# Kernel tuning notes

Hardware: AMD Instinct MI355X
Metric: run time of the kernel (lower is better)

## Reference

```python
import jax, jax.numpy as jnp
import numpy as np

B, L, E, H = 2, 2048, 1024, 16
D = E // H  # head_dim = 64


def setup_inputs() -> dict:
    key = jax.random.key(0)
    ks = jax.random.split(key, 9)
    s = 1.0 / np.sqrt(E)
    return {
        "query": jax.random.normal(ks[0], (B, L, E), jnp.float32),
        "key": jax.random.normal(ks[1], (B, L, E), jnp.float32),
        "value": jax.random.normal(ks[2], (B, L, E), jnp.float32),
        # torch Linear weights are [out_features, in_features]
        "Wq": jax.random.uniform(ks[3], (E, E), jnp.float32, -s, s),
        "bq": jnp.zeros((E,), jnp.float32),
        "Wk": jax.random.uniform(ks[4], (E, E), jnp.float32, -s, s),  # k_proj, no bias (add_bias_kv=False)
        "Wv": jax.random.uniform(ks[5], (E, E), jnp.float32, -s, s),  # v_proj, no bias
        "Wo": jax.random.uniform(ks[6], (E, E), jnp.float32, -s, s),
        "bo": jnp.zeros((E,), jnp.float32),
    }


def reference(query, key, value, Wq, bq, Wk, Wv, Wo, bo):
    # Projections (torch Linear: y = x @ W.T + b)
    q = query @ Wq.T + bq          # [B, L, E]
    k = key @ Wk.T                 # [B, L, E]
    v = value @ Wv.T               # [B, L, E]
    # Split heads
    q = q.reshape(B, L, H, D)
    k = k.reshape(B, L, H, D)
    v = v.reshape(B, L, H, D)
    # Scaled dot-product attention; the source's chunked online-softmax
    # computes exactly softmax(q k^T / sqrt(D)) v.
    q = q / jnp.sqrt(jnp.asarray(D, q.dtype))
    scores = jnp.einsum("bqhd,bkhd->bhqk", q, k)      # [B, H, L, L]
    probs = jax.nn.softmax(scores, axis=-1)
    out = jnp.einsum("bhqk,bkhd->bqhd", probs, v)     # [B, L, H, D]
    out = out.reshape(B, L, E)
    return out @ Wo.T + bo
```

## Files before the change

### kernel.cpp

```cpp
#include <hip/hip_runtime.h>

typedef __bf16 bf16;
typedef __bf16 bf16x8 __attribute__((ext_vector_type(8)));
typedef __bf16 bf16x4 __attribute__((ext_vector_type(4)));
typedef float  f32x4  __attribute__((ext_vector_type(4)));

#define MFMA_BF16(a, b, c) __builtin_amdgcn_mfma_f32_16x16x32_bf16((a), (b), (c), 0, 0, 0)


__device__ __forceinline__ void async_load16(const bf16* g, const bf16* l) {
    auto gp = (const __attribute__((address_space(1))) unsigned int*)(unsigned long long)(const void*)g;
    auto lp = (__attribute__((address_space(3))) unsigned int*)(unsigned int)(unsigned long long)(const void*)l;
    __builtin_amdgcn_global_load_lds(gp, lp, 16, 0, 0);
}

__global__ void cvt_bf16_kernel(
    const float* __restrict__ s0, const float* __restrict__ s1, const float* __restrict__ s2,
    const float* __restrict__ s3, const float* __restrict__ s4, const float* __restrict__ s5,
    const float* __restrict__ s6,
    bf16* __restrict__ d0, bf16* __restrict__ d1, bf16* __restrict__ d2,
    bf16* __restrict__ d3, bf16* __restrict__ d4, bf16* __restrict__ d5,
    bf16* __restrict__ d6)
{
    const float* src; bf16* dst; int n;
    switch (blockIdx.y) {
        case 0: src = s0; dst = d0; n = 4194304; break;
        case 1: src = s1; dst = d1; n = 4194304; break;
        case 2: src = s2; dst = d2; n = 4194304; break;
        case 3: src = s3; dst = d3; n = 1048576; break;
        case 4: src = s4; dst = d4; n = 1048576; break;
        case 5: src = s5; dst = d5; n = 1048576; break;
        default: src = s6; dst = d6; n = 1048576; break;
    }
    int i = (blockIdx.x * 256 + threadIdx.x) * 4;
    if (i >= n) return;
    float4 f = *(const float4*)(src + i);
    bf16x4 o;
    o.x = (bf16)f.x; o.y = (bf16)f.y; o.z = (bf16)f.z; o.w = (bf16)f.w;
    *(bf16x4*)(dst + i) = o;
}

__global__ __launch_bounds__(256, 2) void gemm4_kernel(
    const bf16* __restrict__ Aq, const bf16* __restrict__ Ak, const bf16* __restrict__ Av,
    const bf16* __restrict__ Ao,
    const bf16* __restrict__ Wq, const bf16* __restrict__ Wk, const bf16* __restrict__ Wv,
    const bf16* __restrict__ Wo,
    const float* __restrict__ bq, const float* __restrict__ bo,
    bf16* __restrict__ Qs, bf16* __restrict__ Ksw, bf16* __restrict__ Vsw,
    float* __restrict__ out, int zbase)
{
    const int z = zbase + blockIdx.z;
    const bf16 *A, *W;
    if (z == 0)      { A = Aq; W = Wq; }
    else if (z == 1) { A = Ak; W = Wk; }
    else if (z == 2) { A = Av; W = Wv; }
    else             { A = Ao; W = Wo; }

    __shared__ __align__(16) bf16 lA[128 * 32];
    __shared__ __align__(16) bf16 lB[128 * 32];

    const int tid  = threadIdx.x;
    const int w    = tid >> 6;
    const int lane = tid & 63;
    const int lm   = lane & 15;
    const int g    = lane >> 4;
    const int m0   = blockIdx.y * 128;
    const int n0   = blockIdx.x * 128;
    const int wm   = (w & 1) * 64;
    const int wn   = (w >> 1) * 64;

    f32x4 acc[4][4] = {};
    const int sbase = w * 128 + lane;

    for (int kb = 0; kb < 32; kb++) {
        __syncthreads();
#pragma unroll
        for (int t = 0; t < 2; t++) {
            int s   = sbase + t * 64;
            int row = s >> 2;
            int gs  = s & 3;
            int gg  = gs ^ ((row >> 1) & 3);
            const bf16* ga = A + (size_t)(m0 + row) * 1024 + kb * 32 + gg * 8;
            const bf16* gb = W + (size_t)(n0 + row) * 1024 + kb * 32 + gg * 8;
            async_load16(ga, lA + s * 8);
            async_load16(gb, lB + s * 8);
        }
        __syncthreads();

        bf16x8 af[4], bfr[4];
#pragma unroll
        for (int mt = 0; mt < 4; mt++) {
            int row = wm + mt * 16 + lm;
            af[mt] = *(const bf16x8*)(lA + row * 32 + ((g ^ ((row >> 1) & 3)) << 3));
        }
#pragma unroll
        for (int nt = 0; nt < 4; nt++) {
            int row = wn + nt * 16 + lm;
            bfr[nt] = *(const bf16x8*)(lB + row * 32 + ((g ^ ((row >> 1) & 3)) << 3));
        }
#pragma unroll
        for (int mt = 0; mt < 4; mt++)
#pragma unroll
            for (int nt = 0; nt < 4; nt++)
                acc[mt][nt] = MFMA_BF16(af[mt], bfr[nt], acc[mt][nt]);
    }

    const float scale = (z == 0) ? 0.18033688011112042f : 1.0f;
    const float* bias = (z == 0) ? bq : ((z == 3) ? bo : nullptr);
#pragma unroll
    for (int nt = 0; nt < 4; nt++) {
        int n = n0 + wn + nt * 16 + lm;
        float bv = bias ? bias[n] : 0.0f;
#pragma unroll
        for (int mt = 0; mt < 4; mt++) {
#pragma unroll
            for (int r = 0; r < 4; r++) {
                int m = m0 + wm + mt * 16 + g * 4 + r;
                float val = (acc[mt][nt][r] + bv) * scale;
                if (z == 3) {
                    out[(size_t)m * 1024 + n] = val;
                } else {
                    int b = m >> 11, lpos = m & 2047, h = n >> 6, d = n & 63;
                    size_t hb = (size_t)(b * 16 + h) * (2048 * 64);
                    if (z == 0) {
                        Qs[hb + (size_t)lpos * 64 + d] = (bf16)val;
                    } else if (z == 1) {
                        int kb2 = lpos >> 6, rem = lpos & 63;
                        int c   = ((rem >> 4) & 2) | ((rem >> 2) & 1);
                        int lmk = ((rem >> 1) & 12) | (rem & 3);
                        int f   = d >> 5, gk = (d >> 3) & 3, j = d & 7;
                        Ksw[hb + (size_t)((kb2 * 8 + c * 2 + f) * 64 + gk * 16 + lmk) * 8 + j] = (bf16)val;
                    } else {
                        int kb2 = lpos >> 6, kc = (lpos >> 5) & 1, gv = (lpos >> 3) & 3, j = lpos & 7;
                        int mt2 = d >> 4, lmv = d & 15;
                        Vsw[hb + (size_t)((kb2 * 8 + mt2 * 2 + kc) * 64 + gv * 16 + lmv) * 8 + j] = (bf16)val;
                    }
                }
            }
        }
    }
}

__global__ __launch_bounds__(128, 2) void attn_kernel(
    const bf16* __restrict__ Qs, const bf16* __restrict__ Ksw,
    const bf16* __restrict__ Vsw, bf16* __restrict__ attn)
{
    const int lane = threadIdx.x & 63;
    const int lm   = lane & 15;
    const int g    = lane >> 4;
    const int i    = blockIdx.x;
    const int bh   = ((i & 7) << 2) | ((i >> 3) & 3);
    const int q0   = (i >> 5) * 64 + (threadIdx.x >> 6) * 32;

    const bf16* Qh = Qs  + (size_t)bh * (2048 * 64);
    const bf16* kp = Ksw + (size_t)bh * (2048 * 64) + (size_t)lane * 8;
    const bf16* vp = Vsw + (size_t)bh * (2048 * 64) + (size_t)lane * 8;

    bf16x8 qf[2][2];
#pragma unroll
    for (int qi = 0; qi < 2; qi++)
#pragma unroll
        for (int f = 0; f < 2; f++)
            qf[qi][f] = *(const bf16x8*)(Qh + (size_t)(q0 + qi * 16 + lm) * 64 + f * 32 + g * 8);

    bf16x8 ones;
#pragma unroll
    for (int j = 0; j < 8; j++) ones[j] = (bf16)1.0f;

    f32x4 o[2][4] = {};
    f32x4 lacc[2] = {};

    bf16x8 kf[4][2];
#pragma unroll
    for (int c = 0; c < 4; c++)
#pragma unroll
        for (int f = 0; f < 2; f++)
            kf[c][f] = *(const bf16x8*)(kp + (c * 2 + f) * 512);

    for (int kb = 0; kb < 32; kb++) {
        f32x4 s[2][4] = {};
#pragma unroll
        for (int c = 0; c < 4; c++)
#pragma unroll
            for (int f = 0; f < 2; f++) {
                s[0][c] = MFMA_BF16(kf[c][f], qf[0][f], s[0][c]);
                s[1][c] = MFMA_BF16(kf[c][f], qf[1][f], s[1][c]);
            }

        bf16x8 vf[4][2];
#pragma unroll
        for (int mt = 0; mt < 4; mt++)
#pragma unroll
            for (int kc = 0; kc < 2; kc++)
                vf[mt][kc] = *(const bf16x8*)(vp + (mt * 2 + kc) * 512);
        vp += 4096;

        kp += 4096;
        if (kb < 31) {
#pragma unroll
            for (int c = 0; c < 4; c++)
#pragma unroll
                for (int f = 0; f < 2; f++)
                    kf[c][f] = *(const bf16x8*)(kp + (c * 2 + f) * 512);
        }

        bf16x8 pb[2][2];
#pragma unroll
        for (int qi = 0; qi < 2; qi++)
#pragma unroll
            for (int kc = 0; kc < 2; kc++)
#pragma unroll
                for (int r = 0; r < 4; r++) {
                    pb[qi][kc][r]     = (bf16)exp2f(s[qi][2 * kc][r]);
                    pb[qi][kc][r + 4] = (bf16)exp2f(s[qi][2 * kc + 1][r]);
                }

#pragma unroll
        for (int kc = 0; kc < 2; kc++) {
            lacc[0] = MFMA_BF16(ones, pb[0][kc], lacc[0]);
            lacc[1] = MFMA_BF16(ones, pb[1][kc], lacc[1]);
#pragma unroll
            for (int mt = 0; mt < 4; mt++) {
                o[0][mt] = MFMA_BF16(vf[mt][kc], pb[0][kc], o[0][mt]);
                o[1][mt] = MFMA_BF16(vf[mt][kc], pb[1][kc], o[1][mt]);
            }
        }
    }

    const int b = bh >> 4, h = bh & 15;
#pragma unroll
    for (int qi = 0; qi < 2; qi++) {
        float inv = 1.0f / lacc[qi][0];
        bf16* orow = attn + ((size_t)(b * 2048 + q0 + qi * 16 + lm)) * 1024 + h * 64;
#pragma unroll
        for (int mt = 0; mt < 4; mt++) {
            bf16x4 ov;
#pragma unroll
            for (int r = 0; r < 4; r++) ov[r] = (bf16)(o[qi][mt][r] * inv);
            *(bf16x4*)(orow + mt * 16 + g * 4) = ov;
        }
    }
}

extern "C" void kernel_launch(void* const* d_in, const int* in_sizes, int n_in,
                              void* d_out, int out_size, void* d_ws, size_t ws_size,
                              hipStream_t stream) {
    const float* query = (const float*)d_in[0];
    const float* key   = (const float*)d_in[1];
    const float* value = (const float*)d_in[2];
    const float* Wq    = (const float*)d_in[3];
    const float* bq    = (const float*)d_in[4];
    const float* Wk    = (const float*)d_in[5];
    const float* Wv    = (const float*)d_in[6];
    const float* Wo    = (const float*)d_in[7];
    const float* bo    = (const float*)d_in[8];

    char* ws = (char*)d_ws;
    bf16* Xq  = (bf16*)(ws);
    bf16* Xk  = (bf16*)(ws + ((size_t)8  << 20));
    bf16* Xv  = (bf16*)(ws + ((size_t)16 << 20));
    bf16* Wqb = (bf16*)(ws + ((size_t)24 << 20));
    bf16* Wkb = (bf16*)(ws + ((size_t)26 << 20));
    bf16* Wvb = (bf16*)(ws + ((size_t)28 << 20));
    bf16* Wob = (bf16*)(ws + ((size_t)30 << 20));
    bf16* Qs  = (bf16*)(ws + ((size_t)32 << 20));
    bf16* Ksw = (bf16*)(ws + ((size_t)40 << 20));
    bf16* Vsw = (bf16*)(ws + ((size_t)48 << 20));
    bf16* attn = Xq;

    cvt_bf16_kernel<<<dim3(4096, 7, 1), 256, 0, stream>>>(
        query, key, value, Wq, Wk, Wv, Wo, Xq, Xk, Xv, Wqb, Wkb, Wvb, Wob);

    gemm4_kernel<<<dim3(8, 32, 3), 256, 0, stream>>>(
        Xq, Xk, Xv, attn, Wqb, Wkb, Wvb, Wob, bq, bo, Qs, Ksw, Vsw, (float*)d_out, 0);

    attn_kernel<<<dim3(1024, 1, 1), 128, 0, stream>>>(Qs, Ksw, Vsw, attn);

    gemm4_kernel<<<dim3(8, 32, 1), 256, 0, stream>>>(
        Xq, Xk, Xv, attn, Wqb, Wkb, Wvb, Wob, bq, bo, Qs, Ksw, Vsw, (float*)d_out, 3);
}
```

Measured before the change: 237.3 us.

## Split attention keys across two waves and reduce partial outputs in LDS

Each block now handles 32 queries instead of 64, and its two waves each process half of the key sequence for the same queries. The partial outputs and row sums are combined through shared memory before normalisation. The grid doubles to 2048 blocks and the launch-bounds occupancy hint rises to 4. This is meant to give more parallelism and shorter per-wave loops that hide latency better. In exchange it adds an LDS reduction and a barrier, leaves one wave idle during the epilogue, and makes each query fragment load twice. The softmax has no max subtraction, and splitting keys stays exact because both halves share the same implicit zero reference.

```diff
diff --git a/kernel.cpp b/kernel.cpp
--- a/kernel.cpp
+++ b/kernel.cpp
@@ -141,20 +141,21 @@
     }
 }
 
-__global__ __launch_bounds__(128, 2) void attn_kernel(
+__global__ __launch_bounds__(128, 4) void attn_kernel(
     const bf16* __restrict__ Qs, const bf16* __restrict__ Ksw,
     const bf16* __restrict__ Vsw, bf16* __restrict__ attn)
 {
+    const int w    = threadIdx.x >> 6;
     const int lane = threadIdx.x & 63;
     const int lm   = lane & 15;
     const int g    = lane >> 4;
     const int i    = blockIdx.x;
     const int bh   = ((i & 7) << 2) | ((i >> 3) & 3);
-    const int q0   = (i >> 5) * 64 + (threadIdx.x >> 6) * 32;
+    const int q0   = (i >> 5) * 32;
 
     const bf16* Qh = Qs  + (size_t)bh * (2048 * 64);
-    const bf16* kp = Ksw + (size_t)bh * (2048 * 64) + (size_t)lane * 8;
-    const bf16* vp = Vsw + (size_t)bh * (2048 * 64) + (size_t)lane * 8;
+    const bf16* kp = Ksw + (size_t)bh * (2048 * 64) + (size_t)(w * 16) * 4096 + (size_t)lane * 8;
+    const bf16* vp = Vsw + (size_t)bh * (2048 * 64) + (size_t)(w * 16) * 4096 + (size_t)lane * 8;
 
     bf16x8 qf[2][2];
 #pragma unroll
@@ -177,7 +178,7 @@
         for (int f = 0; f < 2; f++)
             kf[c][f] = *(const bf16x8*)(kp + (c * 2 + f) * 512);
 
-    for (int kb = 0; kb < 32; kb++) {
+    for (int kb = 0; kb < 16; kb++) {
         f32x4 s[2][4] = {};
 #pragma unroll
         for (int c = 0; c < 4; c++)
@@ -196,7 +197,7 @@
         vp += 4096;
 
         kp += 4096;
-        if (kb < 31) {
+        if (kb < 15) {
 #pragma unroll
             for (int c = 0; c < 4; c++)
 #pragma unroll
@@ -227,17 +228,43 @@
         }
     }
 
-    const int b = bh >> 4, h = bh & 15;
-#pragma unroll
-    for (int qi = 0; qi < 2; qi++) {
-        float inv = 1.0f / lacc[qi][0];
-        bf16* orow = attn + ((size_t)(b * 2048 + q0 + qi * 16 + lm)) * 1024 + h * 64;
-#pragma unroll
-        for (int mt = 0; mt < 4; mt++) {
-            bf16x4 ov;
-#pragma unroll
-            for (int r = 0; r < 4; r++) ov[r] = (bf16)(o[qi][mt][r] * inv);
-            *(bf16x4*)(orow + mt * 16 + g * 4) = ov;
+    __shared__ float part[64 * 36];
+    if (w == 1) {
+        float* p = part + lane * 36;
+#pragma unroll
+        for (int qi = 0; qi < 2; qi++)
+#pragma unroll
+            for (int mt = 0; mt < 4; mt++)
+                *(f32x4*)(p + (qi * 4 + mt) * 4) = o[qi][mt];
+        p[32] = lacc[0][0];
+        p[33] = lacc[1][0];
+    }
+    __syncthreads();
+    if (w == 0) {
+        const float* p = part + lane * 36;
+#pragma unroll
+        for (int qi = 0; qi < 2; qi++)
+#pragma unroll
+            for (int mt = 0; mt < 4; mt++) {
+                f32x4 t = *(const f32x4*)(p + (qi * 4 + mt) * 4);
+#pragma unroll
+                for (int r = 0; r < 4; r++) o[qi][mt][r] += t[r];
+            }
+        float ltot0 = lacc[0][0] + p[32];
+        float ltot1 = lacc[1][0] + p[33];
+
+        const int b = bh >> 4, h = bh & 15;
+#pragma unroll
+        for (int qi = 0; qi < 2; qi++) {
+            float inv = 1.0f / (qi == 0 ? ltot0 : ltot1);
+            bf16* orow = attn + ((size_t)(b * 2048 + q0 + qi * 16 + lm)) * 1024 + h * 64;
+#pragma unroll
+            for (int mt = 0; mt < 4; mt++) {
+                bf16x4 ov;
+#pragma unroll
+                for (int r = 0; r < 4; r++) ov[r] = (bf16)(o[qi][mt][r] * inv);
+                *(bf16x4*)(orow + mt * 16 + g * 4) = ov;
+            }
         }
     }
 }
@@ -274,7 +301,7 @@
     gemm4_kernel<<<dim3(8, 32, 3), 256, 0, stream>>>(
         Xq, Xk, Xv, attn, Wqb, Wkb, Wvb, Wob, bq, bo, Qs, Ksw, Vsw, (float*)d_out, 0);
 
-    attn_kernel<<<dim3(1024, 1, 1), 128, 0, stream>>>(Qs, Ksw, Vsw, attn);
+    attn_kernel<<<dim3(2048, 1, 1), 128, 0, stream>>>(Qs, Ksw, Vsw, attn);
 
     gemm4_kernel<<<dim3(8, 32, 1), 256, 0, stream>>>(
         Xq, Xk, Xv, attn, Wqb, Wkb, Wvb, Wob, bq, bo, Qs, Ksw, Vsw, (float*)d_out, 3);
```

Measured after the change: 241.1 us. No clear change (+1.6%).
